# Kernel optimization log

Measured on AMD Instinct MI355X. Metric: run time of the kernel, lower is better.

Reference implementation:

```python
import jax, jax.numpy as jnp
import numpy as np

N_NODES = 100000
N_EDGES = 1600000
D_IN = 128
HID = 64
N_LAYERS = 5
D_OUT = 32
N_GRAPHS = 1000


def setup_inputs() -> dict:
    key = jax.random.key(0)
    ks = jax.random.split(key, 12)
    node_embed = jax.random.normal(ks[0], (N_NODES, D_IN), dtype=jnp.float32)
    edge_index = jax.random.randint(ks[1], (2, N_EDGES), 0, N_NODES, dtype=jnp.int32)
    batch = jnp.sort(jax.random.randint(ks[2], (N_NODES,), 0, N_GRAPHS, dtype=jnp.int32))
    s = 0.1  # weight scale
    return {
        "node_embed": node_embed,
        "edge_index": edge_index,
        "batch": batch,
        "W_in": s * jax.random.normal(ks[3], (D_IN, HID), dtype=jnp.float32),
        "b_in": s * jax.random.normal(ks[4], (HID,), dtype=jnp.float32),
        "ggnn_w": s * jax.random.normal(ks[5], (N_LAYERS, HID, HID), dtype=jnp.float32),
        "gru_w_ih": s * jax.random.normal(ks[6], (3 * HID, HID), dtype=jnp.float32),
        "gru_w_hh": s * jax.random.normal(ks[7], (3 * HID, HID), dtype=jnp.float32),
        "gru_b_ih": s * jax.random.normal(ks[8], (3 * HID,), dtype=jnp.float32),
        "gru_b_hh": s * jax.random.normal(ks[9], (3 * HID,), dtype=jnp.float32),
        "W_out": s * jax.random.normal(ks[10], (HID, D_OUT), dtype=jnp.float32),
        "b_out": s * jax.random.normal(ks[11], (D_OUT,), dtype=jnp.float32),
    }


def _gru_cell(m, h, w_ih, w_hh, b_ih, b_hh):
    # torch.nn.GRUCell: gates ordered (r, z, n)
    gi = m @ w_ih.T + b_ih   # [N, 3H]
    gh = h @ w_hh.T + b_hh   # [N, 3H]
    i_r, i_z, i_n = jnp.split(gi, 3, axis=-1)
    h_r, h_z, h_n = jnp.split(gh, 3, axis=-1)
    r = jax.nn.sigmoid(i_r + h_r)
    z = jax.nn.sigmoid(i_z + h_z)
    n = jnp.tanh(i_n + r * h_n)
    return (1.0 - z) * n + z * h


def reference(node_embed, edge_index, batch, W_in, b_in, ggnn_w,
              gru_w_ih, gru_w_hh, gru_b_ih, gru_b_hh, W_out, b_out):
    n_nodes = node_embed.shape[0]
    src, dst = edge_index[0], edge_index[1]

    # input linear: [N, D_IN] -> [N, H]
    x = node_embed @ W_in + b_in

    # GatedGraphConv: per-layer linear message, add-aggregate, shared GRU update
    def layer(h, w):
        m = h @ w                                   # [N, H]
        agg = jax.ops.segment_sum(m[src], dst, num_segments=n_nodes)  # scatter-add
        h_new = _gru_cell(agg, h, gru_w_ih, gru_w_hh, gru_b_ih, gru_b_hh)
        return h_new, None

    x, _ = jax.lax.scan(layer, x, ggnn_w)

    # global mean pool over graphs
    sums = jax.ops.segment_sum(x, batch, num_segments=N_GRAPHS)       # [G, H]
    cnts = jax.ops.segment_sum(jnp.ones((n_nodes,), x.dtype), batch, num_segments=N_GRAPHS)
    pooled = sums / jnp.maximum(cnts, 1.0)[:, None]

    # dropout is identity in eval mode
    return pooled @ W_out + b_out
```

## Files before the change

kernel.cpp:

```cpp
#include <hip/hip_runtime.h>

#define N_NODES 100000
#define N_EDGES 1600000
#define D_IN 128
#define HID 64
#define N_LAYERS 5
#define D_OUT 32
#define N_GRAPHS 1000

#define BSHIFT 7
#define NBUCK ((N_NODES + 127) >> BSHIFT)
#define CNT_B 256
#define EPB (N_EDGES / CNT_B)
#define NT (NBUCK * CNT_B)

typedef unsigned short ushort_t;
typedef unsigned int uint_t;
typedef __attribute__((ext_vector_type(8))) short short8;
typedef __attribute__((ext_vector_type(4))) float f32x4;

#define MFMA(a, b, c) __builtin_amdgcn_mfma_f32_16x16x32_bf16((a), (b), (c), 0, 0, 0)

#define WSTRIDE (24 * 2 * 64 * 8)
#define NW (N_LAYERS * WSTRIDE)
#define WIN_N (4 * 4 * 64 * 8)

#define IN_B ((N_NODES + 63) / 64)
#define CTOT (CNT_B + IN_B)

__device__ __forceinline__ float fast_sigmoid(float x) {
    return __builtin_amdgcn_rcpf(1.0f + __expf(-x));
}
__device__ __forceinline__ float fast_tanh(float x) {
    return 1.0f - 2.0f * __builtin_amdgcn_rcpf(1.0f + __expf(2.0f * x));
}
__device__ __forceinline__ ushort_t f2bf(float f) {
    uint_t u = __float_as_uint(f);
    return (ushort_t)((u + 0x7fffu + ((u >> 16) & 1u)) >> 16);
}
__device__ __forceinline__ float b2f(ushort_t u) {
    return __uint_as_float(((uint_t)u) << 16);
}
__device__ __forceinline__ void split8(const float* p, short8& hi, short8& lo) {
    float4 u0 = *(const float4*)p;
    float4 u1 = *(const float4*)(p + 4);
#define SPL(ii, fv) { float f_ = (fv); ushort_t h_ = f2bf(f_); hi[ii] = (short)h_;          \
                      float r_ = f_ - __uint_as_float(((uint_t)h_) << 16); lo[ii] = (short)f2bf(r_); }
    SPL(0, u0.x) SPL(1, u0.y) SPL(2, u0.z) SPL(3, u0.w)
    SPL(4, u1.x) SPL(5, u1.y) SPL(6, u1.z) SPL(7, u1.w)
#undef SPL
}

__global__ void k_prep(const float* __restrict__ ggnn_w,
                       const float* __restrict__ w_ih,
                       const float* __restrict__ w_hh,
                       const float* __restrict__ W_in,
                       short* __restrict__ Whi, short* __restrict__ Wlo,
                       short* __restrict__ WinHi, short* __restrict__ WinLo,
                       float* __restrict__ sums, int* __restrict__ done) {
    int t = blockIdx.x * blockDim.x + threadIdx.x;
    if (t == 0) *done = 0;
    if (t < N_GRAPHS * (HID + 1)) sums[t] = 0.0f;
    if (t < NW) {
        int i    = t & 7;
        int lane = (t >> 3) & 63;
        int s    = (t >> 9) & 1;
        int tt   = (t >> 10) % 24;
        int lay  = (t >> 10) / 24;
        int k    = s * 32 + (lane >> 4) * 8 + i;
        int col  = tt * 16 + (lane & 15);
        float val;
        if (col < 192) {
            const float* wl = ggnn_w + ((size_t)lay * HID + k) * HID;
            const float* wi = w_ih + (size_t)col * HID;
            float acc = 0.0f;
#pragma unroll 8
            for (int q = 0; q < HID; ++q) acc = fmaf(wl[q], wi[q], acc);
            val = acc;
        } else {
            val = w_hh[(size_t)(col - 192) * HID + k];
        }
        ushort_t h_ = f2bf(val);
        Whi[t] = (short)h_;
        Wlo[t] = (short)f2bf(val - b2f(h_));
        return;
    }
    int t2 = t - NW;
    if (t2 >= WIN_N) return;
    int i    = t2 & 7;
    int lane = (t2 >> 3) & 63;
    int jb   = (t2 >> 9) & 3;
    int s    = (t2 >> 11) & 3;
    int k    = s * 32 + (lane >> 4) * 8 + i;
    int col  = jb * 16 + (lane & 15);
    float val = W_in[(size_t)k * HID + col];
    ushort_t h_ = f2bf(val);
    WinHi[t2] = (short)h_;
    WinLo[t2] = (short)f2bf(val - b2f(h_));
}

__global__ __launch_bounds__(256) void k_cntin(
        const int* __restrict__ ei, int* __restrict__ table,
        const float* __restrict__ ne,
        const short* __restrict__ WinHi, const short* __restrict__ WinLo,
        const float* __restrict__ b_in,
        ushort_t* __restrict__ hbhi) {
    __shared__ int hcnt[NBUCK];
    int tid = threadIdx.x;
    int swz = (int)(((long long)blockIdx.x * 256) % CTOT);

    if (swz < CNT_B) {
        int b = swz;
        for (int i = tid; i < NBUCK; i += 256) hcnt[i] = 0;
        __syncthreads();
        int e0 = b * EPB;
        for (int i = tid; i < EPB; i += 256)
            atomicAdd(&hcnt[ei[N_EDGES + e0 + i] >> BSHIFT], 1);
        __syncthreads();
        for (int i = tid; i < NBUCK; i += 256)
            table[i * CNT_B + b] = hcnt[i];
        return;
    }
    int ib = swz - CNT_B;
    int wv = tid >> 6, l = tid & 63;
    int q = l >> 4, c = l & 15;
    int nodeBase = ib * 64 + wv * 16;
    int anode = nodeBase + c;
    int acl = (anode < N_NODES) ? anode : (N_NODES - 1);
    const float* erow = ne + (size_t)acl * D_IN;
    short8 Ah[4], Al[4];
#pragma unroll
    for (int s = 0; s < 4; ++s) split8(erow + s * 32 + q * 8, Ah[s], Al[s]);

    f32x4 acc[4];
    const f32x4 zero = {0.f, 0.f, 0.f, 0.f};
#pragma unroll
    for (int jb = 0; jb < 4; ++jb) acc[jb] = zero;
    const short8* BH = ((const short8*)WinHi) + l;
    const short8* BL = ((const short8*)WinLo) + l;
#pragma unroll
    for (int jb = 0; jb < 4; ++jb)
#pragma unroll
        for (int s = 0; s < 4; ++s) {
            short8 bh = BH[(s * 4 + jb) * 64];
            short8 bl = BL[(s * 4 + jb) * 64];
            acc[jb] = MFMA(Ah[s], bh, acc[jb]);
            acc[jb] = MFMA(Al[s], bh, acc[jb]);
            acc[jb] = MFMA(Ah[s], bl, acc[jb]);
        }
#pragma unroll
    for (int jb = 0; jb < 4; ++jb) {
        int j = jb * 16 + c;
        float bb = b_in[j];
#pragma unroll
        for (int i = 0; i < 4; ++i) {
            int m = nodeBase + q * 4 + i;
            if (m < N_NODES)
                hbhi[(size_t)m * HID + j] = f2bf(acc[jb][i] + bb);
        }
    }
}

#define SCHUNK 1024
__global__ __launch_bounds__(1024) void k_tscan1(int* __restrict__ table,
                                                 int* __restrict__ bsum,
                                                 int* __restrict__ done) {
    __shared__ int buf[SCHUNK];
    __shared__ int lastFlag;
    int tid = threadIdx.x;
    int i = blockIdx.x * SCHUNK + tid;
    int v = (i < NT) ? table[i] : 0;
    buf[tid] = v;
    __syncthreads();
    for (int s = 1; s < SCHUNK; s <<= 1) {
        int a = (tid >= s) ? buf[tid - s] : 0;
        __syncthreads();
        buf[tid] += a;
        __syncthreads();
    }
    if (i < NT) table[i] = buf[tid] - v;
    if (tid == SCHUNK - 1) atomicExch(&bsum[blockIdx.x], buf[tid]);
    if (tid == 0) {
        __threadfence();
        lastFlag = (atomicAdd(done, 1) == (int)gridDim.x - 1) ? 1 : 0;
    }
    __syncthreads();
    if (!lastFlag) return;
    int nch = gridDim.x;
    int bv = (tid < nch) ? atomicAdd(&bsum[tid], 0) : 0;
    buf[tid] = bv;
    __syncthreads();
    for (int s = 1; s < SCHUNK; s <<= 1) {
        int a = (tid >= s) ? buf[tid - s] : 0;
        __syncthreads();
        buf[tid] += a;
        __syncthreads();
    }
    if (tid < nch) atomicExch(&bsum[tid], buf[tid] - bv);
}

__global__ __launch_bounds__(256) void k_scatter(const int* __restrict__ ei,
                                                 const int* __restrict__ table,
                                                 const int* __restrict__ bsum,
                                                 uint_t* __restrict__ eb) {
    __shared__ uint2 stage[EPB];
    __shared__ int hoff[NBUCK];
    __shared__ int hslot[NBUCK];
    __shared__ int sbuf[256];
    int b = blockIdx.x, tid = threadIdx.x;
    for (int i = tid; i < NBUCK; i += 256) { hoff[i] = 0; hslot[i] = 0; }
    __syncthreads();
    int e0 = b * EPB;
    for (int i = tid; i < EPB; i += 256)
        atomicAdd(&hoff[ei[N_EDGES + e0 + i] >> BSHIFT], 1);
    __syncthreads();
    int base = tid * 4;
    int c0 = (base + 0 < NBUCK) ? hoff[base + 0] : 0;
    int c1 = (base + 1 < NBUCK) ? hoff[base + 1] : 0;
    int c2 = (base + 2 < NBUCK) ? hoff[base + 2] : 0;
    int c3 = (base + 3 < NBUCK) ? hoff[base + 3] : 0;
    int tot = c0 + c1 + c2 + c3;
    sbuf[tid] = tot;
    __syncthreads();
    for (int s = 1; s < 256; s <<= 1) {
        int a = (tid >= s) ? sbuf[tid - s] : 0;
        __syncthreads();
        sbuf[tid] += a;
        __syncthreads();
    }
    int mybase = sbuf[tid] - tot;
    __syncthreads();
    if (base + 0 < NBUCK) hoff[base + 0] = mybase;
    if (base + 1 < NBUCK) hoff[base + 1] = mybase + c0;
    if (base + 2 < NBUCK) hoff[base + 2] = mybase + c0 + c1;
    if (base + 3 < NBUCK) hoff[base + 3] = mybase + c0 + c1 + c2;
    __syncthreads();
    for (int i = tid; i < EPB; i += 256) {
        int s = ei[e0 + i];
        int d = ei[N_EDGES + e0 + i];
        int bk = d >> BSHIFT;
        int pos = hoff[bk] + atomicAdd(&hslot[bk], 1);
        uint2 v; v.x = (uint_t)s; v.y = (uint_t)d;
        stage[pos] = v;
    }
    __syncthreads();
    for (int p = tid; p < EPB; p += 256) {
        uint2 e = stage[p];
        int bk = (int)e.y >> BSHIFT;
        int gidx = bk * CNT_B + b;
        int gbase = table[gidx] + bsum[gidx >> 10];
        eb[gbase + (p - hoff[bk])] = e.x | ((e.y & 127u) << 17);
    }
}

__global__ __launch_bounds__(256) void k_csr(const int* __restrict__ table,
                                             const int* __restrict__ bsum,
                                             const uint_t* __restrict__ eb,
                                             int* __restrict__ csr,
                                             int* __restrict__ off) {
    __shared__ int cnt[128];
    __shared__ int slot[128];
    int b = blockIdx.x, tid = threadIdx.x;
    int nodeBase = b << BSHIFT;
    int nn = min(128, N_NODES - nodeBase);
    int i0 = b * CNT_B;
    int beg = table[i0] + bsum[i0 >> 10];
    int end;
    if (b == NBUCK - 1) end = N_EDGES;
    else {
        int i1 = (b + 1) * CNT_B;
        end = table[i1] + bsum[i1 >> 10];
    }

    if (tid < 128) { cnt[tid] = 0; slot[tid] = 0; }
    __syncthreads();
    for (int i = beg + tid; i < end; i += 256)
        atomicAdd(&cnt[(eb[i] >> 17) & 127u], 1);
    __syncthreads();
    int orig = (tid < 128) ? cnt[tid] : 0;
    for (int s = 1; s < 128; s <<= 1) {
        int a = (tid >= s && tid < 128) ? cnt[tid - s] : 0;
        __syncthreads();
        if (tid < 128) cnt[tid] += a;
        __syncthreads();
    }
    int start = 0;
    if (tid < 128) start = beg + cnt[tid] - orig;
    __syncthreads();
    if (tid < 128) {
        cnt[tid] = start;
        if (tid < nn) off[nodeBase + tid] = start;
    }
    if (b == NBUCK - 1 && tid == 0) off[N_NODES] = N_EDGES;
    __syncthreads();
    for (int i = beg + tid; i < end; i += 256) {
        uint_t e = eb[i];
        int ln = (e >> 17) & 127u;
        int p = cnt[ln] + atomicAdd(&slot[ln], 1);
        csr[p] = (int)(e & 0x1FFFFu);
    }
}

__global__ __launch_bounds__(256) void k_gather(const int* __restrict__ off,
                                                const int* __restrict__ csr,
                                                const ushort_t* __restrict__ hb,
                                                ushort_t* __restrict__ aggb) {
    int t = blockIdx.x * blockDim.x + threadIdx.x;
    int n = t >> 6;
    int lane = t & 63;
    int q = lane >> 3, c = lane & 7;
    int beg = off[n], end = off[n + 1];
    float a[8];
#pragma unroll
    for (int x = 0; x < 8; ++x) a[x] = 0.f;
#pragma unroll 2
    for (int i = beg; i < end; i += 8) {
        int idx = i + q;
        int sidx = csr[min(idx, end - 1)];
        float msk = (idx < end) ? 1.0f : 0.0f;
        uint4 v = *(const uint4*)(hb + (size_t)sidx * HID + c * 8);
        a[0] = fmaf(msk, __uint_as_float(v.x << 16), a[0]);
        a[1] = fmaf(msk, __uint_as_float(v.x & 0xffff0000u), a[1]);
        a[2] = fmaf(msk, __uint_as_float(v.y << 16), a[2]);
        a[3] = fmaf(msk, __uint_as_float(v.y & 0xffff0000u), a[3]);
        a[4] = fmaf(msk, __uint_as_float(v.z << 16), a[4]);
        a[5] = fmaf(msk, __uint_as_float(v.z & 0xffff0000u), a[5]);
        a[6] = fmaf(msk, __uint_as_float(v.w << 16), a[6]);
        a[7] = fmaf(msk, __uint_as_float(v.w & 0xffff0000u), a[7]);
    }
#pragma unroll
    for (int x = 0; x < 8; ++x) {
        a[x] += __shfl_xor(a[x], 8);
        a[x] += __shfl_xor(a[x], 16);
        a[x] += __shfl_xor(a[x], 32);
    }
    if (q == 0) {
        uint4 o;
        o.x = (uint_t)f2bf(a[0]) | ((uint_t)f2bf(a[1]) << 16);
        o.y = (uint_t)f2bf(a[2]) | ((uint_t)f2bf(a[3]) << 16);
        o.z = (uint_t)f2bf(a[4]) | ((uint_t)f2bf(a[5]) << 16);
        o.w = (uint_t)f2bf(a[6]) | ((uint_t)f2bf(a[7]) << 16);
        *(uint4*)(aggb + (size_t)n * HID + c * 8) = o;
    }
}

__global__ __launch_bounds__(256) void k_gru(const ushort_t* __restrict__ aggb,
                                             ushort_t* __restrict__ hbhi,
                                             const short* __restrict__ Whi,
                                             const short* __restrict__ Wlo,
                                             const float* __restrict__ b_ih,
                                             const float* __restrict__ b_hh) {
    int tid = threadIdx.x;
    int wv = tid >> 6, l = tid & 63;
    int q = l >> 4, c = l & 15;
    int nodeBase = blockIdx.x * 64 + wv * 16;

    int anode = nodeBase + c;
    int acl = (anode < N_NODES) ? anode : (N_NODES - 1);
    const ushort_t* arow = aggb + (size_t)acl * HID;
    const ushort_t* hrow = hbhi + (size_t)acl * HID;
    short8 Ag[2], Ah[2];
    Ag[0] = *(const short8*)(arow + q * 8);
    Ag[1] = *(const short8*)(arow + 32 + q * 8);
    Ah[0] = *(const short8*)(hrow + q * 8);
    Ah[1] = *(const short8*)(hrow + 32 + q * 8);

    const short8* BH = ((const short8*)Whi) + l;
    const short8* BL = ((const short8*)Wlo) + l;
    const f32x4 zero = {0.f, 0.f, 0.f, 0.f};

#pragma unroll
    for (int jb = 0; jb < 4; ++jb) {
        f32x4 acc6[6];
#pragma unroll
        for (int g = 0; g < 6; ++g) acc6[g] = zero;
#pragma unroll
        for (int g = 0; g < 6; ++g) {
            int t = g * 4 + jb;
            short8 b0h = BH[(t * 2 + 0) * 64];
            short8 b1h = BH[(t * 2 + 1) * 64];
            short8 a0 = (g < 3) ? Ag[0] : Ah[0];
            short8 a1 = (g < 3) ? Ag[1] : Ah[1];
            acc6[g] = MFMA(a0, b0h, acc6[g]);
            acc6[g] = MFMA(a1, b1h, acc6[g]);
            if (g == 2 || g == 5) {
                short8 b0l = BL[(t * 2 + 0) * 64];
                short8 b1l = BL[(t * 2 + 1) * 64];
                acc6[g] = MFMA(a0, b0l, acc6[g]);
                acc6[g] = MFMA(a1, b1l, acc6[g]);
            }
        }
        int j = jb * 16 + c;
        float br  = b_ih[j] + b_hh[j];
        float bz  = b_ih[64 + j] + b_hh[64 + j];
        float bin = b_ih[128 + j];
        float bhn = b_hh[128 + j];
#pragma unroll
        for (int i = 0; i < 4; ++i) {
            int m = nodeBase + q * 4 + i;
            if (m < N_NODES) {
                float rr = fast_sigmoid(acc6[0][i] + acc6[3][i] + br);
                float zz = fast_sigmoid(acc6[1][i] + acc6[4][i] + bz);
                float nv = fast_tanh((acc6[2][i] + bin) + rr * (acc6[5][i] + bhn));
                size_t idx = (size_t)m * HID + j;
                float hold = b2f(hbhi[idx]);
                hbhi[idx] = f2bf((1.0f - zz) * nv + zz * hold);
            }
        }
    }
}

#define POOL_NPW 32
__global__ void k_pool(const ushort_t* __restrict__ hb,
                       const int* __restrict__ batch,
                       float* __restrict__ sums,
                       float* __restrict__ cntf) {
    int wid = (blockIdx.x * blockDim.x + threadIdx.x) >> 6;
    int j = threadIdx.x & 63;
    int base = wid * POOL_NPW;
    if (base >= N_NODES) return;
    int end = base + POOL_NPW;
    if (end > N_NODES) end = N_NODES;
    float acc = 0.f, c = 0.f;
    int curg = batch[base];
    for (int n = base; n < end; ++n) {
        int g = batch[n];
        if (g != curg) {
            atomicAdd(&sums[(size_t)curg * HID + j], acc);
            if (j == 0) atomicAdd(&cntf[curg], c);
            acc = 0.f; c = 0.f; curg = g;
        }
        acc += b2f(hb[(size_t)n * HID + j]);
        c += 1.f;
    }
    atomicAdd(&sums[(size_t)curg * HID + j], acc);
    if (j == 0) atomicAdd(&cntf[curg], c);
}

__global__ void k_out(const float* __restrict__ sums,
                      const float* __restrict__ cntf,
                      const float* __restrict__ W_out,
                      const float* __restrict__ b_out,
                      float* __restrict__ out) {
    int t = blockIdx.x * blockDim.x + threadIdx.x;
    if (t >= N_GRAPHS * D_OUT) return;
    int g = t / D_OUT, o = t % D_OUT;
    float inv_c = __builtin_amdgcn_rcpf(fmaxf(cntf[g], 1.0f));
    float acc = 0.0f;
#pragma unroll
    for (int k = 0; k < HID; ++k)
        acc = fmaf(sums[g * HID + k], W_out[k * D_OUT + o], acc);
    out[t] = acc * inv_c + b_out[o];
}

static inline char* align256(char* p) {
    return (char*)(((uintptr_t)p + 255) & ~(uintptr_t)255);
}

extern "C" void kernel_launch(void* const* d_in, const int* in_sizes, int n_in,
                              void* d_out, int out_size, void* d_ws, size_t ws_size,
                              hipStream_t stream) {
    const float* node_embed = (const float*)d_in[0];
    const int*   edge_index = (const int*)  d_in[1];
    const int*   batch      = (const int*)  d_in[2];
    const float* W_in       = (const float*)d_in[3];
    const float* b_in       = (const float*)d_in[4];
    const float* ggnn_w     = (const float*)d_in[5];
    const float* gru_w_ih   = (const float*)d_in[6];
    const float* gru_w_hh   = (const float*)d_in[7];
    const float* gru_b_ih   = (const float*)d_in[8];
    const float* gru_b_hh   = (const float*)d_in[9];
    const float* W_out      = (const float*)d_in[10];
    const float* b_out      = (const float*)d_in[11];
    float* out = (float*)d_out;

    char* p = (char*)d_ws;
    ushort_t* hbhi  = (ushort_t*)p; p = align256(p + (size_t)N_NODES * HID * sizeof(ushort_t));
    ushort_t* aggb  = (ushort_t*)p; p = align256(p + (size_t)N_NODES * HID * sizeof(ushort_t));
    int*      csr   = (int*)p;      p = align256(p + (size_t)N_EDGES * sizeof(int));
    uint_t*   eb    = (uint_t*)p;   p = align256(p + (size_t)N_EDGES * sizeof(uint_t));
    int*      table = (int*)p;      p = align256(p + (size_t)NT * sizeof(int));
    int*      off   = (int*)p;      p = align256(p + (size_t)(N_NODES + 1) * sizeof(int));
    int*      bsumT = (int*)p;      p = align256(p + 256 * sizeof(int));
    int*      doneT = (int*)p;      p = align256(p + 256 * sizeof(int));
    short*    Whi   = (short*)p;    p = align256(p + (size_t)NW * sizeof(short));
    short*    Wlo   = (short*)p;    p = align256(p + (size_t)NW * sizeof(short));
    short*    WinHi = (short*)p;    p = align256(p + (size_t)WIN_N * sizeof(short));
    short*    WinLo = (short*)p;    p = align256(p + (size_t)WIN_N * sizeof(short));
    float*    sums  = (float*)p;
    float*    cntf  = (float*)(p + (size_t)N_GRAPHS * HID * sizeof(float));

    const int BLK = 256;
    const int nchunksT = (NT + SCHUNK - 1) / SCHUNK;

    k_prep<<<(NW + WIN_N) / BLK, BLK, 0, stream>>>(
        ggnn_w, gru_w_ih, gru_w_hh, W_in, Whi, Wlo, WinHi, WinLo, sums, doneT);

    k_cntin<<<CTOT, BLK, 0, stream>>>(
        edge_index, table, node_embed, WinHi, WinLo, b_in, hbhi);

    k_tscan1<<<nchunksT, SCHUNK, 0, stream>>>(table, bsumT, doneT);
    k_scatter<<<CNT_B, BLK, 0, stream>>>(edge_index, table, bsumT, eb);
    k_csr<<<NBUCK, BLK, 0, stream>>>(table, bsumT, eb, csr, off);

    for (int l = 0; l < N_LAYERS; ++l) {
        k_gather<<<N_NODES * 64 / BLK, BLK, 0, stream>>>(off, csr, hbhi, aggb);
        k_gru<<<(N_NODES + 63) / 64, BLK, 0, stream>>>(
            aggb, hbhi, Whi + (size_t)l * WSTRIDE, Wlo + (size_t)l * WSTRIDE,
            gru_b_ih, gru_b_hh);
    }

    {
        int waves = (N_NODES + POOL_NPW - 1) / POOL_NPW;
        int threads = waves * 64;
        k_pool<<<(threads + BLK - 1) / BLK, BLK, 0, stream>>>(hbhi, batch, sums, cntf);
    }
    k_out<<<(N_GRAPHS * D_OUT + BLK - 1) / BLK, BLK, 0, stream>>>(sums, cntf, W_out, b_out, out);
}
```

Baseline: 398.7 us.

## Fuse neighbor gather with GRU update into one per-layer kernel

Merges the gather kernel and the GRU kernel into one k_layer kernel. Each wave gathers 16 nodes serially into shared memory, then runs the MFMA GRU update from LDS, ping-ponging between two hidden-state buffers. This removes the aggregate buffer's global write and read and one launch per layer. The cost is far less gather parallelism: each wave now walks 16 nodes one after another instead of one node per wave, which may expose memory latency.

```diff
diff --git a/kernel.cpp b/kernel.cpp
--- a/kernel.cpp
+++ b/kernel.cpp
@@ -104,7 +104,7 @@
         const float* __restrict__ ne,
         const short* __restrict__ WinHi, const short* __restrict__ WinLo,
         const float* __restrict__ b_in,
-        ushort_t* __restrict__ hbhi) {
+        ushort_t* __restrict__ h0) {
     __shared__ int hcnt[NBUCK];
     int tid = threadIdx.x;
     int swz = (int)(((long long)blockIdx.x * 256) % CTOT);
@@ -156,7 +156,7 @@
         for (int i = 0; i < 4; ++i) {
             int m = nodeBase + q * 4 + i;
             if (m < N_NODES)
-                hbhi[(size_t)m * HID + j] = f2bf(acc[jb][i] + bb);
+                h0[(size_t)m * HID + j] = f2bf(acc[jb][i] + bb);
         }
     }
 }
@@ -301,72 +301,69 @@
     }
 }
 
-__global__ __launch_bounds__(256) void k_gather(const int* __restrict__ off,
-                                                const int* __restrict__ csr,
-                                                const ushort_t* __restrict__ hb,
-                                                ushort_t* __restrict__ aggb) {
-    int t = blockIdx.x * blockDim.x + threadIdx.x;
-    int n = t >> 6;
-    int lane = t & 63;
-    int q = lane >> 3, c = lane & 7;
-    int beg = off[n], end = off[n + 1];
-    float a[8];
-#pragma unroll
-    for (int x = 0; x < 8; ++x) a[x] = 0.f;
+__global__ __launch_bounds__(256) void k_layer(
+        const int* __restrict__ off, const int* __restrict__ csr,
+        const ushort_t* __restrict__ hold_, ushort_t* __restrict__ hnew,
+        const short* __restrict__ Whi, const short* __restrict__ Wlo,
+        const float* __restrict__ b_ih, const float* __restrict__ b_hh) {
+    __shared__ ushort_t sA[4][16][64];
+    int tid = threadIdx.x;
+    int wv = tid >> 6, lane = tid & 63;
+    int nodeBase = blockIdx.x * 64 + wv * 16;
+
+    {
+        int q = lane >> 3, c = lane & 7;
+        for (int m = 0; m < 16; ++m) {
+            int n = nodeBase + m;
+            if (n >= N_NODES) break;
+            int beg = off[n], end = off[n + 1];
+            float a[8];
+#pragma unroll
+            for (int x = 0; x < 8; ++x) a[x] = 0.f;
 #pragma unroll 2
-    for (int i = beg; i < end; i += 8) {
-        int idx = i + q;
-        int sidx = csr[min(idx, end - 1)];
-        float msk = (idx < end) ? 1.0f : 0.0f;
-        uint4 v = *(const uint4*)(hb + (size_t)sidx * HID + c * 8);
-        a[0] = fmaf(msk, __uint_as_float(v.x << 16), a[0]);
-        a[1] = fmaf(msk, __uint_as_float(v.x & 0xffff0000u), a[1]);
-        a[2] = fmaf(msk, __uint_as_float(v.y << 16), a[2]);
-        a[3] = fmaf(msk, __uint_as_float(v.y & 0xffff0000u), a[3]);
-        a[4] = fmaf(msk, __uint_as_float(v.z << 16), a[4]);
-        a[5] = fmaf(msk, __uint_as_float(v.z & 0xffff0000u), a[5]);
-        a[6] = fmaf(msk, __uint_as_float(v.w << 16), a[6]);
-        a[7] = fmaf(msk, __uint_as_float(v.w & 0xffff0000u), a[7]);
-    }
-#pragma unroll
-    for (int x = 0; x < 8; ++x) {
-        a[x] += __shfl_xor(a[x], 8);
-        a[x] += __shfl_xor(a[x], 16);
-        a[x] += __shfl_xor(a[x], 32);
-    }
-    if (q == 0) {
-        uint4 o;
-        o.x = (uint_t)f2bf(a[0]) | ((uint_t)f2bf(a[1]) << 16);
-        o.y = (uint_t)f2bf(a[2]) | ((uint_t)f2bf(a[3]) << 16);
-        o.z = (uint_t)f2bf(a[4]) | ((uint_t)f2bf(a[5]) << 16);
-        o.w = (uint_t)f2bf(a[6]) | ((uint_t)f2bf(a[7]) << 16);
-        *(uint4*)(aggb + (size_t)n * HID + c * 8) = o;
-    }
-}
-
-__global__ __launch_bounds__(256) void k_gru(const ushort_t* __restrict__ aggb,
-                                             ushort_t* __restrict__ hbhi,
-                                             const short* __restrict__ Whi,
-                                             const short* __restrict__ Wlo,
-                                             const float* __restrict__ b_ih,
-                                             const float* __restrict__ b_hh) {
-    int tid = threadIdx.x;
-    int wv = tid >> 6, l = tid & 63;
-    int q = l >> 4, c = l & 15;
-    int nodeBase = blockIdx.x * 64 + wv * 16;
-
+            for (int i = beg; i < end; i += 8) {
+                int idx = i + q;
+                int sidx = csr[min(idx, end - 1)];
+                float msk = (idx < end) ? 1.0f : 0.0f;
+                uint4 v = *(const uint4*)(hold_ + (size_t)sidx * HID + c * 8);
+                a[0] = fmaf(msk, __uint_as_float(v.x << 16), a[0]);
+                a[1] = fmaf(msk, __uint_as_float(v.x & 0xffff0000u), a[1]);
+                a[2] = fmaf(msk, __uint_as_float(v.y << 16), a[2]);
+                a[3] = fmaf(msk, __uint_as_float(v.y & 0xffff0000u), a[3]);
+                a[4] = fmaf(msk, __uint_as_float(v.z << 16), a[4]);
+                a[5] = fmaf(msk, __uint_as_float(v.z & 0xffff0000u), a[5]);
+                a[6] = fmaf(msk, __uint_as_float(v.w << 16), a[6]);
+                a[7] = fmaf(msk, __uint_as_float(v.w & 0xffff0000u), a[7]);
+            }
+#pragma unroll
+            for (int x = 0; x < 8; ++x) {
+                a[x] += __shfl_xor(a[x], 8);
+                a[x] += __shfl_xor(a[x], 16);
+                a[x] += __shfl_xor(a[x], 32);
+            }
+            if (q == 0) {
+                uint4 o;
+                o.x = (uint_t)f2bf(a[0]) | ((uint_t)f2bf(a[1]) << 16);
+                o.y = (uint_t)f2bf(a[2]) | ((uint_t)f2bf(a[3]) << 16);
+                o.z = (uint_t)f2bf(a[4]) | ((uint_t)f2bf(a[5]) << 16);
+                o.w = (uint_t)f2bf(a[6]) | ((uint_t)f2bf(a[7]) << 16);
+                *(uint4*)&sA[wv][m][c * 8] = o;
+            }
+        }
+    }
+
+    int q = lane >> 4, c = lane & 15;
     int anode = nodeBase + c;
     int acl = (anode < N_NODES) ? anode : (N_NODES - 1);
-    const ushort_t* arow = aggb + (size_t)acl * HID;
-    const ushort_t* hrow = hbhi + (size_t)acl * HID;
+    const ushort_t* hrow = hold_ + (size_t)acl * HID;
     short8 Ag[2], Ah[2];
-    Ag[0] = *(const short8*)(arow + q * 8);
-    Ag[1] = *(const short8*)(arow + 32 + q * 8);
+    Ag[0] = *(const short8*)&sA[wv][c][q * 8];
+    Ag[1] = *(const short8*)&sA[wv][c][32 + q * 8];
     Ah[0] = *(const short8*)(hrow + q * 8);
     Ah[1] = *(const short8*)(hrow + 32 + q * 8);
 
-    const short8* BH = ((const short8*)Whi) + l;
-    const short8* BL = ((const short8*)Wlo) + l;
+    const short8* BH = ((const short8*)Whi) + lane;
+    const short8* BL = ((const short8*)Wlo) + lane;
     const f32x4 zero = {0.f, 0.f, 0.f, 0.f};
 
 #pragma unroll
@@ -403,8 +400,8 @@
                 float zz = fast_sigmoid(acc6[1][i] + acc6[4][i] + bz);
                 float nv = fast_tanh((acc6[2][i] + bin) + rr * (acc6[5][i] + bhn));
                 size_t idx = (size_t)m * HID + j;
-                float hold = b2f(hbhi[idx]);
-                hbhi[idx] = f2bf((1.0f - zz) * nv + zz * hold);
+                float hov = b2f(hold_[idx]);
+                hnew[idx] = f2bf((1.0f - zz) * nv + zz * hov);
             }
         }
     }
@@ -475,8 +472,8 @@
     float* out = (float*)d_out;
 
     char* p = (char*)d_ws;
-    ushort_t* hbhi  = (ushort_t*)p; p = align256(p + (size_t)N_NODES * HID * sizeof(ushort_t));
-    ushort_t* aggb  = (ushort_t*)p; p = align256(p + (size_t)N_NODES * HID * sizeof(ushort_t));
+    ushort_t* h0    = (ushort_t*)p; p = align256(p + (size_t)N_NODES * HID * sizeof(ushort_t));
+    ushort_t* h1    = (ushort_t*)p; p = align256(p + (size_t)N_NODES * HID * sizeof(ushort_t));
     int*      csr   = (int*)p;      p = align256(p + (size_t)N_EDGES * sizeof(int));
     uint_t*   eb    = (uint_t*)p;   p = align256(p + (size_t)N_EDGES * sizeof(uint_t));
     int*      table = (int*)p;      p = align256(p + (size_t)NT * sizeof(int));
@@ -497,23 +494,25 @@
         ggnn_w, gru_w_ih, gru_w_hh, W_in, Whi, Wlo, WinHi, WinLo, sums, doneT);
 
     k_cntin<<<CTOT, BLK, 0, stream>>>(
-        edge_index, table, node_embed, WinHi, WinLo, b_in, hbhi);
+        edge_index, table, node_embed, WinHi, WinLo, b_in, h0);
 
     k_tscan1<<<nchunksT, SCHUNK, 0, stream>>>(table, bsumT, doneT);
     k_scatter<<<CNT_B, BLK, 0, stream>>>(edge_index, table, bsumT, eb);
     k_csr<<<NBUCK, BLK, 0, stream>>>(table, bsumT, eb, csr, off);
 
+    ushort_t* hin = h0;
+    ushort_t* hout = h1;
     for (int l = 0; l < N_LAYERS; ++l) {
-        k_gather<<<N_NODES * 64 / BLK, BLK, 0, stream>>>(off, csr, hbhi, aggb);
-        k_gru<<<(N_NODES + 63) / 64, BLK, 0, stream>>>(
-            aggb, hbhi, Whi + (size_t)l * WSTRIDE, Wlo + (size_t)l * WSTRIDE,
+        k_layer<<<(N_NODES + 63) / 64, BLK, 0, stream>>>(
+            off, csr, hin, hout, Whi + (size_t)l * WSTRIDE, Wlo + (size_t)l * WSTRIDE,
             gru_b_ih, gru_b_hh);
+        ushort_t* t = hin; hin = hout; hout = t;
     }
 
     {
         int waves = (N_NODES + POOL_NPW - 1) / POOL_NPW;
         int threads = waves * 64;
-        k_pool<<<(threads + BLK - 1) / BLK, BLK, 0, stream>>>(hbhi, batch, sums, cntf);
+        k_pool<<<(threads + BLK - 1) / BLK, BLK, 0, stream>>>(hin, batch, sums, cntf);
     }
     k_out<<<(N_GRAPHS * D_OUT + BLK - 1) / BLK, BLK, 0, stream>>>(sums, cntf, W_out, b_out, out);
 }
```

Result: slower. 480.6 us (+20.5%).
